# Kernel tuning notes

Hardware: AMD Instinct MI355X
Metric: run time of the kernel (lower is better)

Reference implementation:

```python
import jax, jax.numpy as jnp
import numpy as np
import math

EMBED = 1024
N_HEAD = 16
T_LEN = 2048
BATCH = 2
MLP_MULT = 4
EPS = 1e-5


def setup_inputs() -> dict:
    key = jax.random.key(0)
    ks = jax.random.split(key, 12)
    d = EMBED
    h = MLP_MULT * d
    s = 0.02
    return {
        "x": jax.random.normal(ks[0], (BATCH, T_LEN, d), dtype=jnp.float32),
        "ln1_scale": jnp.ones((d,), jnp.float32),
        "ln1_shift": jnp.zeros((d,), jnp.float32),
        "w_qkv": jax.random.normal(ks[1], (d, 3 * d), jnp.float32) * s,
        "b_qkv": jnp.zeros((3 * d,), jnp.float32),
        "ln2_scale": jnp.ones((d,), jnp.float32),
        "ln2_shift": jnp.zeros((d,), jnp.float32),
        "w_fc": jax.random.normal(ks[2], (d, h), jnp.float32) * s,
        "b_fc": jnp.zeros((h,), jnp.float32),
        "w_proj": jax.random.normal(ks[3], (h, d), jnp.float32) * s,
        "b_proj": jnp.zeros((d,), jnp.float32),
    }


def _layer_norm(x, scale, shift):
    mu = jnp.mean(x, axis=-1, keepdims=True)
    var = jnp.var(x, axis=-1, keepdims=True)
    return (x - mu) * jax.lax.rsqrt(var + EPS) * scale + shift


def _attention(h, w_qkv, b_qkv):
    B, T, C = h.shape
    hd = C // N_HEAD
    qkv = h @ w_qkv + b_qkv  # [B,T,3C]
    q, k, v = jnp.split(qkv, 3, axis=-1)
    q = q.reshape(B, T, N_HEAD, hd)
    k = k.reshape(B, T, N_HEAD, hd)
    v = v.reshape(B, T, N_HEAD, hd)
    scores = jnp.einsum("bthd,bshd->bhts", q, k) * (1.0 / math.sqrt(hd))
    causal = jnp.tril(jnp.ones((T, T), dtype=bool))
    scores = jnp.where(causal[None, None], scores, -jnp.inf)
    probs = jax.nn.softmax(scores, axis=-1)
    y = jnp.einsum("bhts,bshd->bthd", probs, v)
    return y.reshape(B, T, C)


def reference(x, ln1_scale, ln1_shift, w_qkv, b_qkv, ln2_scale, ln2_shift,
              w_fc, b_fc, w_proj, b_proj):
    x = x + _attention(_layer_norm(x, ln1_scale, ln1_shift), w_qkv, b_qkv)
    h = _layer_norm(x, ln2_scale, ln2_shift)
    # note: module names it 'gelu' but it's nn.ReLU()
    h = jax.nn.relu(h @ w_fc + b_fc) @ w_proj + b_proj
    return x + h
```

## Files before the change

kernel.cpp:

```cpp
#include <hip/hip_runtime.h>
#include <hip/hip_bf16.h>


typedef __bf16  bf16x8  __attribute__((ext_vector_type(8)));
typedef __bf16  bf16x4  __attribute__((ext_vector_type(4)));
typedef float   floatx4 __attribute__((ext_vector_type(4)));

#define T_LEN 2048
#define EMB   1024
#define NH    16
#define HD    64
#define HID   4096

#define GLOBAL_LOAD_LDS16(gp, lp) \
    __builtin_amdgcn_global_load_lds( \
        (const __attribute__((address_space(1))) void*)(gp), \
        (__attribute__((address_space(3))) void*)(lp), 16, 0, 0)

__global__ void transpose_all(const float* __restrict__ w_qkv, __bf16* __restrict__ o_qkv,
                              const float* __restrict__ w_fc,  __bf16* __restrict__ o_fc,
                              const float* __restrict__ w_pj,  __bf16* __restrict__ o_pj) {
    __shared__ float tile[32][33];
    int bid = blockIdx.x;
    const float* in; __bf16* out; int R, C, bx, by;
    if (bid < 3072)      { in = w_qkv; out = o_qkv; R = 1024; C = 3072;
                           int r = bid;        bx = r % 96;  by = r / 96;  }
    else if (bid < 7168) { in = w_fc;  out = o_fc;  R = 1024; C = 4096;
                           int r = bid - 3072; bx = r % 128; by = r / 128; }
    else                 { in = w_pj;  out = o_pj;  R = 4096; C = 1024;
                           int r = bid - 7168; bx = r % 32;  by = r / 32;  }
    int bc = bx * 32, br = by * 32;
    int tx = threadIdx.x, ty = threadIdx.y;
    for (int i = 0; i < 32; i += 8)
        tile[ty + i][tx] = in[(size_t)(br + ty + i) * C + bc + tx];
    __syncthreads();
    for (int i = 0; i < 32; i += 8) {
        int c = bc + ty + i, r = br + tx;
        out[(size_t)c * R + r] = (__bf16)tile[tx][ty + i];
    }
}

__global__ __launch_bounds__(256)
void ln_kernel(const float* __restrict__ in, const float* __restrict__ sc,
               const float* __restrict__ sh, __bf16* __restrict__ out) {
    int row = blockIdx.x;
    const float* p = in + (size_t)row * EMB;
    int tid = threadIdx.x;
    int lane = tid & 63, wave = tid >> 6;
    float v[4];
    float s = 0.f, s2 = 0.f;
    for (int j = 0; j < 4; j++) {
        v[j] = p[tid + j * 256];
        s += v[j]; s2 += v[j] * v[j];
    }
    for (int m = 1; m < 64; m <<= 1) {
        s  += __shfl_xor(s, m);
        s2 += __shfl_xor(s2, m);
    }
    __shared__ float ssum[4], ssum2[4];
    if (lane == 0) { ssum[wave] = s; ssum2[wave] = s2; }
    __syncthreads();
    float tot  = ssum[0] + ssum[1] + ssum[2] + ssum[3];
    float tot2 = ssum2[0] + ssum2[1] + ssum2[2] + ssum2[3];
    float mean = tot * (1.f / EMB);
    float var  = tot2 * (1.f / EMB) - mean * mean;
    float rstd = rsqrtf(var + 1e-5f);
    for (int j = 0; j < 4; j++) {
        int c = tid + j * 256;
        out[(size_t)row * EMB + c] = (__bf16)((v[j] - mean) * rstd * sc[c] + sh[c]);
    }
}

__global__ __launch_bounds__(512)
void gemm256(const __bf16* __restrict__ A, const __bf16* __restrict__ Bt,
             const float* __restrict__ bias, const float* __restrict__ res,
             float* __restrict__ outF, __bf16* __restrict__ outB,
             int M, int N, int lda, int KL, int relu, int gx, int gz) {
    __shared__ __align__(16) __bf16 sA[2][256][64];
    __shared__ __align__(16) __bf16 sB[2][256][64];
    const int BUFE = 256 * 64;
    int tid  = threadIdx.x;
    int lane = tid & 63, wave = tid >> 6;
    int quad = lane >> 4, l16 = lane & 15;

    int i  = blockIdx.x;
    int c  = i & 7, m = i >> 3;
    int bx = m % gx;
    int p  = (m / gx) * 8 + c;
    int by = p / gz;
    int bz = p - by * gz;

    int bm = by * 256, bn = bx * 256;
    size_t k0 = (size_t)bz * KL;
    int wm = (wave >> 2) * 128, wn = (wave & 3) * 64;

    floatx4 acc[8][4] = {};

    int srow  = tid >> 3;
    int sslot = (tid & 7) ^ (srow & 7);
    const __bf16* gA = A  + (size_t)(bm + srow) * lda + k0 + sslot * 8;
    const __bf16* gB = Bt + (size_t)(bn + srow) * lda + k0 + sslot * 8;
    __bf16* lA = &sA[0][0][0] + wave * 512;
    __bf16* lB = &sB[0][0][0] + wave * 512;
    const size_t rstep = (size_t)64 * lda;

#define STAGE256(nb, ko) do { \
    GLOBAL_LOAD_LDS16(gA + (ko),             lA + (nb) * BUFE); \
    GLOBAL_LOAD_LDS16(gB + (ko),             lB + (nb) * BUFE); \
    GLOBAL_LOAD_LDS16(gA + (ko) + rstep,     lA + (nb) * BUFE + 4096); \
    GLOBAL_LOAD_LDS16(gB + (ko) + rstep,     lB + (nb) * BUFE + 4096); \
    GLOBAL_LOAD_LDS16(gA + (ko) + 2 * rstep, lA + (nb) * BUFE + 8192); \
    GLOBAL_LOAD_LDS16(gB + (ko) + 2 * rstep, lB + (nb) * BUFE + 8192); \
    GLOBAL_LOAD_LDS16(gA + (ko) + 3 * rstep, lA + (nb) * BUFE + 12288); \
    GLOBAL_LOAD_LDS16(gB + (ko) + 3 * rstep, lB + (nb) * BUFE + 12288); \
} while (0)

#define PHASE_BAR_IN()  do { __builtin_amdgcn_s_barrier(); \
    asm volatile("s_waitcnt lgkmcnt(0)" ::: "memory"); \
    __builtin_amdgcn_sched_barrier(0); } while (0)
#define PHASE_BAR_OUT() do { __builtin_amdgcn_s_barrier(); \
    asm volatile("" ::: "memory"); } while (0)

    STAGE256(0, (size_t)0);

    int xs0  = ((quad) ^ (l16 & 7)) * 8;
    int xs1  = ((4 + quad) ^ (l16 & 7)) * 8;
    int aoff = (wm + l16) * 64;
    int boff = (wn + l16) * 64;

    const int nt = KL / 64;
    for (int t = 0; t < nt; ++t) {
        const int cur = t & 1;
        __builtin_amdgcn_s_barrier();
        asm volatile("" ::: "memory");
        if (t + 1 < nt) {
            STAGE256(cur ^ 1, (size_t)(t + 1) * 64);
            asm volatile("s_waitcnt vmcnt(8)" ::: "memory");
        } else {
            asm volatile("s_waitcnt vmcnt(0)" ::: "memory");
        }
        __builtin_amdgcn_s_barrier();
        asm volatile("" ::: "memory");
        __builtin_amdgcn_sched_barrier(0);

        const __bf16* sAc = &sA[0][0][0] + cur * BUFE;
        const __bf16* sBc = &sB[0][0][0] + cur * BUFE;

        bf16x8 a0[4][2], a1[4][2], b0[2][2], b1[2][2];

        #pragma unroll
        for (int mi = 0; mi < 4; ++mi) {
            a0[mi][0] = *(const bf16x8*)(sAc + aoff + mi * 1024 + xs0);
            a0[mi][1] = *(const bf16x8*)(sAc + aoff + mi * 1024 + xs1);
        }
        #pragma unroll
        for (int nj = 0; nj < 2; ++nj) {
            b0[nj][0] = *(const bf16x8*)(sBc + boff + nj * 1024 + xs0);
            b0[nj][1] = *(const bf16x8*)(sBc + boff + nj * 1024 + xs1);
        }
        PHASE_BAR_IN();
        __builtin_amdgcn_s_setprio(1);
        #pragma unroll
        for (int ks = 0; ks < 2; ++ks)
            #pragma unroll
            for (int mi = 0; mi < 4; ++mi)
                #pragma unroll
                for (int nj = 0; nj < 2; ++nj)
                    acc[mi][nj] = __builtin_amdgcn_mfma_f32_16x16x32_bf16(
                        a0[mi][ks], b0[nj][ks], acc[mi][nj], 0, 0, 0);
        __builtin_amdgcn_s_setprio(0);
        PHASE_BAR_OUT();

        #pragma unroll
        for (int nj = 0; nj < 2; ++nj) {
            b1[nj][0] = *(const bf16x8*)(sBc + boff + (2 + nj) * 1024 + xs0);
            b1[nj][1] = *(const bf16x8*)(sBc + boff + (2 + nj) * 1024 + xs1);
        }
        PHASE_BAR_IN();
        __builtin_amdgcn_s_setprio(1);
        #pragma unroll
        for (int ks = 0; ks < 2; ++ks)
            #pragma unroll
            for (int mi = 0; mi < 4; ++mi)
                #pragma unroll
                for (int nj = 0; nj < 2; ++nj)
                    acc[mi][2 + nj] = __builtin_amdgcn_mfma_f32_16x16x32_bf16(
                        a0[mi][ks], b1[nj][ks], acc[mi][2 + nj], 0, 0, 0);
        __builtin_amdgcn_s_setprio(0);
        PHASE_BAR_OUT();

        #pragma unroll
        for (int mi = 0; mi < 4; ++mi) {
            a1[mi][0] = *(const bf16x8*)(sAc + aoff + (4 + mi) * 1024 + xs0);
            a1[mi][1] = *(const bf16x8*)(sAc + aoff + (4 + mi) * 1024 + xs1);
        }
        PHASE_BAR_IN();
        __builtin_amdgcn_s_setprio(1);
        #pragma unroll
        for (int ks = 0; ks < 2; ++ks)
            #pragma unroll
            for (int mi = 0; mi < 4; ++mi)
                #pragma unroll
                for (int nj = 0; nj < 2; ++nj)
                    acc[4 + mi][2 + nj] = __builtin_amdgcn_mfma_f32_16x16x32_bf16(
                        a1[mi][ks], b1[nj][ks], acc[4 + mi][2 + nj], 0, 0, 0);
        __builtin_amdgcn_s_setprio(0);
        PHASE_BAR_OUT();

        __builtin_amdgcn_s_setprio(1);
        #pragma unroll
        for (int ks = 0; ks < 2; ++ks)
            #pragma unroll
            for (int mi = 0; mi < 4; ++mi)
                #pragma unroll
                for (int nj = 0; nj < 2; ++nj)
                    acc[4 + mi][nj] = __builtin_amdgcn_mfma_f32_16x16x32_bf16(
                        a1[mi][ks], b0[nj][ks], acc[4 + mi][nj], 0, 0, 0);
        __builtin_amdgcn_s_setprio(0);
    }
#undef STAGE256
#undef PHASE_BAR_IN
#undef PHASE_BAR_OUT

    if (bias) {
        #pragma unroll
        for (int mi = 0; mi < 8; ++mi) {
            int row0 = bm + wm + mi * 16 + quad * 4;
            #pragma unroll
            for (int nj = 0; nj < 4; ++nj) {
                int col = bn + wn + nj * 16 + l16;
                float bv = bias[col];
                #pragma unroll
                for (int r = 0; r < 4; ++r) {
                    size_t idx = (size_t)(row0 + r) * N + col;
                    float cc = acc[mi][nj][r] + bv;
                    if (relu) cc = fmaxf(cc, 0.f);
                    if (res)  cc += res[idx];
                    if (outF) outF[idx] = cc;
                    if (outB) outB[idx] = (__bf16)cc;
                }
            }
        }
    } else {
        __bf16* po = outB + (size_t)bz * M * N;
        #pragma unroll
        for (int mi = 0; mi < 8; ++mi) {
            int row0 = bm + wm + mi * 16 + quad * 4;
            #pragma unroll
            for (int nj = 0; nj < 4; ++nj) {
                int col = bn + wn + nj * 16 + l16;
                #pragma unroll
                for (int r = 0; r < 4; ++r)
                    po[(size_t)(row0 + r) * N + col] = (__bf16)acc[mi][nj][r];
            }
        }
    }
}

__global__ __launch_bounds__(256)
void reduce_proj(const __bf16* __restrict__ pbuf, const float* __restrict__ x2,
                 const float* __restrict__ bias, float* __restrict__ out) {
    const size_t MN = (size_t)4096 * 1024;
    size_t i = (size_t)blockIdx.x * 256 + threadIdx.x;
    float4 r = ((const float4*)x2)[i];
    float4 bb = ((const float4*)bias)[i & 255];
    float acc0 = r.x + bb.x, acc1 = r.y + bb.y;
    float acc2 = r.z + bb.z, acc3 = r.w + bb.w;
    for (int k = 0; k < 4; k++) {
        bf16x4 pv = *(const bf16x4*)&pbuf[k * MN + i * 4];
        acc0 += (float)pv[0]; acc1 += (float)pv[1];
        acc2 += (float)pv[2]; acc3 += (float)pv[3];
    }
    float4 o = {acc0, acc1, acc2, acc3};
    ((float4*)out)[i] = o;
}

__global__ __launch_bounds__(256)
void gemm_bt_n64(const __bf16* __restrict__ A, const __bf16* __restrict__ Bt,
                 const float* __restrict__ bias, const float* __restrict__ res,
                 float* __restrict__ outF, __bf16* __restrict__ outB,
                 int M, int N, int K, int relu) {
    __shared__ __align__(16) __bf16 sA[128][40];
    __shared__ __align__(16) __bf16 sB[64][40];
    int tid  = threadIdx.x;
    int lane = tid & 63, wave = tid >> 6;
    int quad = lane >> 4, l16 = lane & 15;
    int bm = blockIdx.y * 128, bn = blockIdx.x * 64;
    int wm = (wave & 1) * 64, wn = (wave >> 1) * 32;
    floatx4 acc[4][2] = {};

    int srow = tid >> 2;
    int scol = (tid & 3) * 8;
    const __bf16* gA = &A[(size_t)(bm + srow) * K + scol];
    const __bf16* gB = &Bt[(size_t)(bn + srow) * K + scol];

    uint4 ra0 = *(const uint4*)gA;
    uint4 ra1 = *(const uint4*)(gA + (size_t)64 * K);
    uint4 rb0 = *(const uint4*)gB;

    for (int kk = 0; kk < K; kk += 32) {
        __syncthreads();
        *(uint4*)&sA[srow][scol]      = ra0;
        *(uint4*)&sA[srow + 64][scol] = ra1;
        *(uint4*)&sB[srow][scol]      = rb0;
        __syncthreads();
        {
            int kn = (kk + 32 < K) ? kk + 32 : kk;
            ra0 = *(const uint4*)(gA + kn);
            ra1 = *(const uint4*)(gA + kn + (size_t)64 * K);
            rb0 = *(const uint4*)(gB + kn);
        }
        bf16x8 af[4], bfr[2];
        for (int i = 0; i < 4; i++)
            af[i] = *(const bf16x8*)&sA[wm + i * 16 + l16][quad * 8];
        for (int j = 0; j < 2; j++)
            bfr[j] = *(const bf16x8*)&sB[wn + j * 16 + l16][quad * 8];
        for (int i = 0; i < 4; i++)
            for (int j = 0; j < 2; j++)
                acc[i][j] = __builtin_amdgcn_mfma_f32_16x16x32_bf16(
                    af[i], bfr[j], acc[i][j], 0, 0, 0);
    }

    for (int i = 0; i < 4; i++) {
        int row0 = bm + wm + i * 16 + quad * 4;
        for (int j = 0; j < 2; j++) {
            int col = bn + wn + j * 16 + l16;
            float bv = bias[col];
            for (int r = 0; r < 4; r++) {
                size_t idx = (size_t)(row0 + r) * N + col;
                float c = acc[i][j][r] + bv;
                if (relu) c = fmaxf(c, 0.f);
                if (res)  c += res[idx];
                if (outF) outF[idx] = c;
                if (outB) outB[idx] = (__bf16)c;
            }
        }
    }
}

__global__ __launch_bounds__(512)
void attn_kernel(const __bf16* __restrict__ qkv, const float* __restrict__ x,
                 float* __restrict__ x2) {
    __shared__ __align__(16) __bf16 sK[2][64][72];
    __shared__ __align__(16) __bf16 sVt[2][64][72];
    __shared__ __align__(16) __bf16 sP[8][16][72];
    const int tid  = threadIdx.x;
    const int lane = tid & 63, wave = tid >> 6;
    const int quad = lane >> 4, l16 = lane & 15;

    int i = blockIdx.x;
    int c = i & 7, m = i >> 3;
    const int bh   = (m & 3) * 8 + c;
    const int qt_h = 31 - (m >> 2);
    const int h    = bh & (NH - 1);
    const int b    = bh >> 4;
    const size_t rowbase = (size_t)b * T_LEN;

    const int g  = wave >> 2;
    const int wg = wave & 3;
    const int qt = g ? (31 - qt_h) : qt_h;
    const int qrow = qt * 64 + wg * 16;
    const int dt   = qt;

    const float kQScale = 0.125f * 1.44269504088896f;
    bf16x8 ones;
    for (int j = 0; j < 8; j++) ones[j] = (__bf16)1.0f;

    const int key0 = tid >> 3, m8 = tid & 7;
    const __bf16* kp0 = qkv + (rowbase + key0) * 3072 + h * HD + m8 * 8 + 1024;
    const int pc0 = ((key0 >> 3) ^ m8) * 8 + (key0 & 7);

    bf16x8 qf[2];
    for (int ks = 0; ks < 2; ks++) {
        bf16x8 raw = *(const bf16x8*)&qkv[(rowbase + qrow + l16) * 3072
                                          + h * HD + ks * 32 + quad * 8];
        for (int j = 0; j < 8; j++)
            qf[ks][j] = (__bf16)((float)raw[j] * kQScale);
    }

    floatx4 o[4] = {}, ol = {};

    const int ntiles = qt_h + 1;
    const size_t TSTEP = (size_t)64 * 3072;

    uint4 kr0 = *(const uint4*)kp0;
    uint4 vr0 = *(const uint4*)(kp0 + 1024);
    {
        *(uint4*)&sK[0][key0][m8 * 8] = kr0;
        bf16x8 v0 = *(bf16x8*)&vr0;
        for (int j = 0; j < 8; j++) sVt[0][m8 * 8 + j][pc0] = v0[j];
    }
    kr0 = *(const uint4*)(kp0 + TSTEP);
    vr0 = *(const uint4*)(kp0 + TSTEP + 1024);
    __syncthreads();

    for (int kt = 0; kt < ntiles; kt++) {
        const int cur = kt & 1, nxt = cur ^ 1;
        if (kt + 1 < ntiles) {
            *(uint4*)&sK[nxt][key0][m8 * 8] = kr0;
            bf16x8 v0 = *(bf16x8*)&vr0;
            for (int j = 0; j < 8; j++) sVt[nxt][m8 * 8 + j][pc0] = v0[j];
            size_t offn = (size_t)((kt + 2 < ntiles) ? kt + 2 : kt + 1) * TSTEP;
            kr0 = *(const uint4*)(kp0 + offn);
            vr0 = *(const uint4*)(kp0 + offn + 1024);
        }

        if (kt <= dt) {
            floatx4 s_acc[4] = {};
            for (int jt = 0; jt < 4; jt++)
                for (int ks = 0; ks < 2; ks++) {
                    bf16x8 kf = *(const bf16x8*)&sK[cur][jt * 16 + l16]
                                                  [ks * 32 + quad * 8];
                    s_acc[jt] = __builtin_amdgcn_mfma_f32_16x16x32_bf16(
                        qf[ks], kf, s_acc[jt], 0, 0, 0);
                }

            if (kt == dt) {
                const int tq0 = qrow + quad * 4;
                const int k0 = kt * 64;
                for (int jt = 0; jt < 4; jt++) {
                    int key = k0 + jt * 16 + l16;
                    for (int r = 0; r < 4; r++) {
                        float sv = (key <= tq0 + r) ? s_acc[jt][r] : -1e30f;
                        float pv = __builtin_amdgcn_exp2f(fminf(sv, 30.f));
                        sP[wave][quad * 4 + r][jt * 16 + l16] = (__bf16)pv;
                    }
                }
            } else {
                for (int jt = 0; jt < 4; jt++)
                    for (int r = 0; r < 4; r++) {
                        float pv = __builtin_amdgcn_exp2f(fminf(s_acc[jt][r], 30.f));
                        sP[wave][quad * 4 + r][jt * 16 + l16] = (__bf16)pv;
                    }
            }

            for (int kp = 0; kp < 2; kp++) {
                bf16x8 pf = *(const bf16x8*)&sP[wave][l16][kp * 32 + quad * 8];
                ol = __builtin_amdgcn_mfma_f32_16x16x32_bf16(pf, ones, ol, 0, 0, 0);
                for (int jt2 = 0; jt2 < 4; jt2++) {
                    int d = jt2 * 16 + l16;
                    int pg = (kp * 4 + quad) ^ (d >> 3);
                    bf16x8 vf = *(const bf16x8*)&sVt[cur][d][pg * 8];
                    o[jt2] = __builtin_amdgcn_mfma_f32_16x16x32_bf16(
                        pf, vf, o[jt2], 0, 0, 0);
                }
            }
        }
        __syncthreads();
    }

    float inv[4];
    for (int r = 0; r < 4; r++) inv[r] = __builtin_amdgcn_rcpf(ol[r]);
    for (int jt2 = 0; jt2 < 4; jt2++) {
        for (int r = 0; r < 4; r++) {
            int tq  = qrow + quad * 4 + r;
            int col = h * HD + jt2 * 16 + l16;
            size_t gi = (rowbase + tq) * EMB + col;
            x2[gi] = x[gi] + o[jt2][r] * inv[r];
        }
    }
}

extern "C" void kernel_launch(void* const* d_in, const int* in_sizes, int n_in,
                              void* d_out, int out_size, void* d_ws, size_t ws_size,
                              hipStream_t stream) {
    const float* x      = (const float*)d_in[0];
    const float* ln1_s  = (const float*)d_in[1];
    const float* ln1_b  = (const float*)d_in[2];
    const float* w_qkv  = (const float*)d_in[3];
    const float* b_qkv  = (const float*)d_in[4];
    const float* ln2_s  = (const float*)d_in[5];
    const float* ln2_b  = (const float*)d_in[6];
    const float* w_fc   = (const float*)d_in[7];
    const float* b_fc   = (const float*)d_in[8];
    const float* w_proj = (const float*)d_in[9];
    const float* b_proj = (const float*)d_in[10];
    float* out = (float*)d_out;

    const int M = 2 * T_LEN;
    char* ws = (char*)d_ws;
    size_t off = 0;
    auto alloc = [&](size_t bytes) {
        void* p = ws + off; off += (bytes + 255) & ~(size_t)255; return p;
    };
    __bf16* wpj_t  = (__bf16*)alloc((size_t)1024 * 4096 * 2);
    float*  x2     = (float*) alloc((size_t)M * 1024 * 4);
    __bf16* hfc    = (__bf16*)alloc((size_t)M * 4096 * 2);
    size_t mark = off;
    __bf16* wqkv_t = (__bf16*)alloc((size_t)3072 * 1024 * 2);
    __bf16* wfc_t  = (__bf16*)alloc((size_t)4096 * 1024 * 2);
    __bf16* h1     = (__bf16*)alloc((size_t)M * 1024 * 2);
    __bf16* h2     = (__bf16*)alloc((size_t)M * 1024 * 2);
    __bf16* qkvb   = (__bf16*)alloc((size_t)M * 3072 * 2);
    __bf16* pbuf = (__bf16*)(ws + mark);
    size_t need = mark + (size_t)4 * M * 1024 * 2;
    bool can_split = ws_size >= need;

    dim3 tb(32, 8);
    transpose_all<<<11264, tb, 0, stream>>>(w_qkv, wqkv_t, w_fc, wfc_t,
                                            w_proj, wpj_t);

    ln_kernel<<<M, 256, 0, stream>>>(x, ln1_s, ln1_b, h1);

    gemm256<<<192, 512, 0, stream>>>(
        h1, wqkv_t, b_qkv, nullptr, nullptr, qkvb, M, 3072, 1024, 1024, 0,
        12, 1);

    attn_kernel<<<512, 512, 0, stream>>>(qkvb, x, x2);

    ln_kernel<<<M, 256, 0, stream>>>(x2, ln2_s, ln2_b, h2);

    gemm256<<<256, 512, 0, stream>>>(
        h2, wfc_t, b_fc, nullptr, nullptr, hfc, M, 4096, 1024, 1024, 1,
        16, 1);

    if (can_split) {
        gemm256<<<256, 512, 0, stream>>>(
            hfc, wpj_t, nullptr, nullptr, nullptr, pbuf, M, 1024, 4096, 1024, 0,
            4, 4);
        reduce_proj<<<(M * 1024 / 4) / 256, 256, 0, stream>>>(
            pbuf, x2, b_proj, out);
    } else {
        gemm_bt_n64<<<dim3(1024 / 64, M / 128), 256, 0, stream>>>(
            hfc, wpj_t, b_proj, x2, out, nullptr, M, 1024, 4096, 0);
    }
}
```

Before: 314.5 us.

## Replace 256x256 phased GEMM with simpler 128x128 tile, K-step 32 kernel

Swaps the 256x256-tile, 512-thread GEMM and its four-phase barrier/priority scheduling for a 128x128-tile, 256-thread kernel with a 32-wide K step and a new swizzled LDS layout. All three GEMM launches now use four times as many blocks. The aim is better occupancy and load balance across the CUs for these matrix sizes. In exchange there is less data reuse per tile, twice as many K iterations with barriers, and the fine-grained MFMA/LDS interleaving is gone.

```diff
diff --git a/kernel.cpp b/kernel.cpp
--- a/kernel.cpp
+++ b/kernel.cpp
@@ -71,14 +71,13 @@
     }
 }
 
-__global__ __launch_bounds__(512)
-void gemm256(const __bf16* __restrict__ A, const __bf16* __restrict__ Bt,
+__global__ __launch_bounds__(256)
+void gemm128(const __bf16* __restrict__ A, const __bf16* __restrict__ Bt,
              const float* __restrict__ bias, const float* __restrict__ res,
              float* __restrict__ outF, __bf16* __restrict__ outB,
              int M, int N, int lda, int KL, int relu, int gx, int gz) {
-    __shared__ __align__(16) __bf16 sA[2][256][64];
-    __shared__ __align__(16) __bf16 sB[2][256][64];
-    const int BUFE = 256 * 64;
+    __shared__ __align__(16) __bf16 sA[2][4096];
+    __shared__ __align__(16) __bf16 sB[2][4096];
     int tid  = threadIdx.x;
     int lane = tid & 63, wave = tid >> 6;
     int quad = lane >> 4, l16 = lane & 15;
@@ -90,141 +89,70 @@
     int by = p / gz;
     int bz = p - by * gz;
 
-    int bm = by * 256, bn = bx * 256;
+    int bm = by * 128, bn = bx * 128;
     size_t k0 = (size_t)bz * KL;
-    int wm = (wave >> 2) * 128, wn = (wave & 3) * 64;
-
-    floatx4 acc[8][4] = {};
-
-    int srow  = tid >> 3;
-    int sslot = (tid & 7) ^ (srow & 7);
-    const __bf16* gA = A  + (size_t)(bm + srow) * lda + k0 + sslot * 8;
-    const __bf16* gB = Bt + (size_t)(bn + srow) * lda + k0 + sslot * 8;
-    __bf16* lA = &sA[0][0][0] + wave * 512;
-    __bf16* lB = &sB[0][0][0] + wave * 512;
+    int wm = (wave & 1) * 64, wn = (wave >> 1) * 64;
+
+    floatx4 acc[4][4] = {};
+
+    int prow  = tid >> 3, pslot = tid & 7;
+    int sw    = pslot ^ (prow & 7);
+    int srowg = 2 * prow + (sw >> 2);
+    int scolg = (sw & 3) * 8;
+    const __bf16* gA = A  + (size_t)(bm + srowg) * lda + k0 + scolg;
+    const __bf16* gB = Bt + (size_t)(bn + srowg) * lda + k0 + scolg;
+    __bf16* lA = &sA[0][0] + tid * 8;
+    __bf16* lB = &sB[0][0] + tid * 8;
     const size_t rstep = (size_t)64 * lda;
 
-#define STAGE256(nb, ko) do { \
-    GLOBAL_LOAD_LDS16(gA + (ko),             lA + (nb) * BUFE); \
-    GLOBAL_LOAD_LDS16(gB + (ko),             lB + (nb) * BUFE); \
-    GLOBAL_LOAD_LDS16(gA + (ko) + rstep,     lA + (nb) * BUFE + 4096); \
-    GLOBAL_LOAD_LDS16(gB + (ko) + rstep,     lB + (nb) * BUFE + 4096); \
-    GLOBAL_LOAD_LDS16(gA + (ko) + 2 * rstep, lA + (nb) * BUFE + 8192); \
-    GLOBAL_LOAD_LDS16(gB + (ko) + 2 * rstep, lB + (nb) * BUFE + 8192); \
-    GLOBAL_LOAD_LDS16(gA + (ko) + 3 * rstep, lA + (nb) * BUFE + 12288); \
-    GLOBAL_LOAD_LDS16(gB + (ko) + 3 * rstep, lB + (nb) * BUFE + 12288); \
+#define STAGE128(nb, ko) do { \
+    GLOBAL_LOAD_LDS16(gA + (ko),         lA + (nb) * 4096); \
+    GLOBAL_LOAD_LDS16(gB + (ko),         lB + (nb) * 4096); \
+    GLOBAL_LOAD_LDS16(gA + (ko) + rstep, lA + (nb) * 4096 + 2048); \
+    GLOBAL_LOAD_LDS16(gB + (ko) + rstep, lB + (nb) * 4096 + 2048); \
 } while (0)
 
-#define PHASE_BAR_IN()  do { __builtin_amdgcn_s_barrier(); \
-    asm volatile("s_waitcnt lgkmcnt(0)" ::: "memory"); \
-    __builtin_amdgcn_sched_barrier(0); } while (0)
-#define PHASE_BAR_OUT() do { __builtin_amdgcn_s_barrier(); \
-    asm volatile("" ::: "memory"); } while (0)
-
-    STAGE256(0, (size_t)0);
-
-    int xs0  = ((quad) ^ (l16 & 7)) * 8;
-    int xs1  = ((4 + quad) ^ (l16 & 7)) * 8;
-    int aoff = (wm + l16) * 64;
-    int boff = (wn + l16) * 64;
-
-    const int nt = KL / 64;
+    STAGE128(0, (size_t)0);
+
+    int psl  = ((l16 & 1) * 4 + quad) ^ ((l16 >> 1) & 7);
+    int aoff = wm * 32 + (l16 >> 1) * 64 + psl * 8;
+    int boff = wn * 32 + (l16 >> 1) * 64 + psl * 8;
+
+    const int nt = KL / 32;
     for (int t = 0; t < nt; ++t) {
         const int cur = t & 1;
         __builtin_amdgcn_s_barrier();
         asm volatile("" ::: "memory");
         if (t + 1 < nt) {
-            STAGE256(cur ^ 1, (size_t)(t + 1) * 64);
-            asm volatile("s_waitcnt vmcnt(8)" ::: "memory");
+            STAGE128(cur ^ 1, (size_t)(t + 1) * 32);
+            asm volatile("s_waitcnt vmcnt(4)" ::: "memory");
         } else {
             asm volatile("s_waitcnt vmcnt(0)" ::: "memory");
         }
         __builtin_amdgcn_s_barrier();
         asm volatile("" ::: "memory");
-        __builtin_amdgcn_sched_barrier(0);
-
-        const __bf16* sAc = &sA[0][0][0] + cur * BUFE;
-        const __bf16* sBc = &sB[0][0][0] + cur * BUFE;
-
-        bf16x8 a0[4][2], a1[4][2], b0[2][2], b1[2][2];
-
+
+        const __bf16* sAc = &sA[cur][0];
+        const __bf16* sBc = &sB[cur][0];
+        bf16x8 af[4], bfr[4];
+        #pragma unroll
+        for (int mi = 0; mi < 4; ++mi)
+            af[mi] = *(const bf16x8*)(sAc + aoff + mi * 512);
+        #pragma unroll
+        for (int nj = 0; nj < 4; ++nj)
+            bfr[nj] = *(const bf16x8*)(sBc + boff + nj * 512);
+        #pragma unroll
+        for (int mi = 0; mi < 4; ++mi)
+            #pragma unroll
+            for (int nj = 0; nj < 4; ++nj)
+                acc[mi][nj] = __builtin_amdgcn_mfma_f32_16x16x32_bf16(
+                    af[mi], bfr[nj], acc[mi][nj], 0, 0, 0);
+    }
+#undef STAGE128
+
+    if (bias) {
         #pragma unroll
         for (int mi = 0; mi < 4; ++mi) {
-            a0[mi][0] = *(const bf16x8*)(sAc + aoff + mi * 1024 + xs0);
-            a0[mi][1] = *(const bf16x8*)(sAc + aoff + mi * 1024 + xs1);
-        }
-        #pragma unroll
-        for (int nj = 0; nj < 2; ++nj) {
-            b0[nj][0] = *(const bf16x8*)(sBc + boff + nj * 1024 + xs0);
-            b0[nj][1] = *(const bf16x8*)(sBc + boff + nj * 1024 + xs1);
-        }
-        PHASE_BAR_IN();
-        __builtin_amdgcn_s_setprio(1);
-        #pragma unroll
-        for (int ks = 0; ks < 2; ++ks)
-            #pragma unroll
-            for (int mi = 0; mi < 4; ++mi)
-                #pragma unroll
-                for (int nj = 0; nj < 2; ++nj)
-                    acc[mi][nj] = __builtin_amdgcn_mfma_f32_16x16x32_bf16(
-                        a0[mi][ks], b0[nj][ks], acc[mi][nj], 0, 0, 0);
-        __builtin_amdgcn_s_setprio(0);
-        PHASE_BAR_OUT();
-
-        #pragma unroll
-        for (int nj = 0; nj < 2; ++nj) {
-            b1[nj][0] = *(const bf16x8*)(sBc + boff + (2 + nj) * 1024 + xs0);
-            b1[nj][1] = *(const bf16x8*)(sBc + boff + (2 + nj) * 1024 + xs1);
-        }
-        PHASE_BAR_IN();
-        __builtin_amdgcn_s_setprio(1);
-        #pragma unroll
-        for (int ks = 0; ks < 2; ++ks)
-            #pragma unroll
-            for (int mi = 0; mi < 4; ++mi)
-                #pragma unroll
-                for (int nj = 0; nj < 2; ++nj)
-                    acc[mi][2 + nj] = __builtin_amdgcn_mfma_f32_16x16x32_bf16(
-                        a0[mi][ks], b1[nj][ks], acc[mi][2 + nj], 0, 0, 0);
-        __builtin_amdgcn_s_setprio(0);
-        PHASE_BAR_OUT();
-
-        #pragma unroll
-        for (int mi = 0; mi < 4; ++mi) {
-            a1[mi][0] = *(const bf16x8*)(sAc + aoff + (4 + mi) * 1024 + xs0);
-            a1[mi][1] = *(const bf16x8*)(sAc + aoff + (4 + mi) * 1024 + xs1);
-        }
-        PHASE_BAR_IN();
-        __builtin_amdgcn_s_setprio(1);
-        #pragma unroll
-        for (int ks = 0; ks < 2; ++ks)
-            #pragma unroll
-            for (int mi = 0; mi < 4; ++mi)
-                #pragma unroll
-                for (int nj = 0; nj < 2; ++nj)
-                    acc[4 + mi][2 + nj] = __builtin_amdgcn_mfma_f32_16x16x32_bf16(
-                        a1[mi][ks], b1[nj][ks], acc[4 + mi][2 + nj], 0, 0, 0);
-        __builtin_amdgcn_s_setprio(0);
-        PHASE_BAR_OUT();
-
-        __builtin_amdgcn_s_setprio(1);
-        #pragma unroll
-        for (int ks = 0; ks < 2; ++ks)
-            #pragma unroll
-            for (int mi = 0; mi < 4; ++mi)
-                #pragma unroll
-                for (int nj = 0; nj < 2; ++nj)
-                    acc[4 + mi][nj] = __builtin_amdgcn_mfma_f32_16x16x32_bf16(
-                        a1[mi][ks], b0[nj][ks], acc[4 + mi][nj], 0, 0, 0);
-        __builtin_amdgcn_s_setprio(0);
-    }
-#undef STAGE256
-#undef PHASE_BAR_IN
-#undef PHASE_BAR_OUT
-
-    if (bias) {
-        #pragma unroll
-        for (int mi = 0; mi < 8; ++mi) {
             int row0 = bm + wm + mi * 16 + quad * 4;
             #pragma unroll
             for (int nj = 0; nj < 4; ++nj) {
@@ -244,7 +172,7 @@
     } else {
         __bf16* po = outB + (size_t)bz * M * N;
         #pragma unroll
-        for (int mi = 0; mi < 8; ++mi) {
+        for (int mi = 0; mi < 4; ++mi) {
             int row0 = bm + wm + mi * 16 + quad * 4;
             #pragma unroll
             for (int nj = 0; nj < 4; ++nj) {
@@ -502,22 +430,22 @@
 
     ln_kernel<<<M, 256, 0, stream>>>(x, ln1_s, ln1_b, h1);
 
-    gemm256<<<192, 512, 0, stream>>>(
+    gemm128<<<768, 256, 0, stream>>>(
         h1, wqkv_t, b_qkv, nullptr, nullptr, qkvb, M, 3072, 1024, 1024, 0,
-        12, 1);
+        24, 1);
 
     attn_kernel<<<512, 512, 0, stream>>>(qkvb, x, x2);
 
     ln_kernel<<<M, 256, 0, stream>>>(x2, ln2_s, ln2_b, h2);
 
-    gemm256<<<256, 512, 0, stream>>>(
+    gemm128<<<1024, 256, 0, stream>>>(
         h2, wfc_t, b_fc, nullptr, nullptr, hfc, M, 4096, 1024, 1024, 1,
-        16, 1);
+        32, 1);
 
     if (can_split) {
-        gemm256<<<256, 512, 0, stream>>>(
+        gemm128<<<1024, 256, 0, stream>>>(
             hfc, wpj_t, nullptr, nullptr, nullptr, pbuf, M, 1024, 4096, 1024, 0,
-            4, 4);
+            8, 4);
         reduce_proj<<<(M * 1024 / 4) / 256, 256, 0, stream>>>(
             pbuf, x2, b_proj, out);
     } else {
```

After: 322.5 us. +2.6%, slower.

## Software-pipeline attention QK with triple-buffered K/V; drop GEMM phase barriers

Applied to the files above, without the earlier changes.

Attention now keeps three K/V LDS buffers and computes the next tile's QK^T scores while the current tile's softmax and PV run. Global loads are issued two tiles ahead and stored after compute. The aim is to hide LDS and MFMA latency across tiles, at the cost of extra LDS and registers. The GEMM also drops its intra-iteration phase barriers and lgkmcnt waits, leaving the compiler to schedule LDS reads against MFMAs.

```diff
diff --git a/kernel.cpp b/kernel.cpp
--- a/kernel.cpp
+++ b/kernel.cpp
@@ -115,12 +115,6 @@
     GLOBAL_LOAD_LDS16(gB + (ko) + 3 * rstep, lB + (nb) * BUFE + 12288); \
 } while (0)
 
-#define PHASE_BAR_IN()  do { __builtin_amdgcn_s_barrier(); \
-    asm volatile("s_waitcnt lgkmcnt(0)" ::: "memory"); \
-    __builtin_amdgcn_sched_barrier(0); } while (0)
-#define PHASE_BAR_OUT() do { __builtin_amdgcn_s_barrier(); \
-    asm volatile("" ::: "memory"); } while (0)
-
     STAGE256(0, (size_t)0);
 
     int xs0  = ((quad) ^ (l16 & 7)) * 8;
@@ -158,7 +152,6 @@
             b0[nj][0] = *(const bf16x8*)(sBc + boff + nj * 1024 + xs0);
             b0[nj][1] = *(const bf16x8*)(sBc + boff + nj * 1024 + xs1);
         }
-        PHASE_BAR_IN();
         __builtin_amdgcn_s_setprio(1);
         #pragma unroll
         for (int ks = 0; ks < 2; ++ks)
@@ -169,14 +162,12 @@
                     acc[mi][nj] = __builtin_amdgcn_mfma_f32_16x16x32_bf16(
                         a0[mi][ks], b0[nj][ks], acc[mi][nj], 0, 0, 0);
         __builtin_amdgcn_s_setprio(0);
-        PHASE_BAR_OUT();
 
         #pragma unroll
         for (int nj = 0; nj < 2; ++nj) {
             b1[nj][0] = *(const bf16x8*)(sBc + boff + (2 + nj) * 1024 + xs0);
             b1[nj][1] = *(const bf16x8*)(sBc + boff + (2 + nj) * 1024 + xs1);
         }
-        PHASE_BAR_IN();
         __builtin_amdgcn_s_setprio(1);
         #pragma unroll
         for (int ks = 0; ks < 2; ++ks)
@@ -187,14 +178,12 @@
                     acc[mi][2 + nj] = __builtin_amdgcn_mfma_f32_16x16x32_bf16(
                         a0[mi][ks], b1[nj][ks], acc[mi][2 + nj], 0, 0, 0);
         __builtin_amdgcn_s_setprio(0);
-        PHASE_BAR_OUT();
 
         #pragma unroll
         for (int mi = 0; mi < 4; ++mi) {
             a1[mi][0] = *(const bf16x8*)(sAc + aoff + (4 + mi) * 1024 + xs0);
             a1[mi][1] = *(const bf16x8*)(sAc + aoff + (4 + mi) * 1024 + xs1);
         }
-        PHASE_BAR_IN();
         __builtin_amdgcn_s_setprio(1);
         #pragma unroll
         for (int ks = 0; ks < 2; ++ks)
@@ -205,7 +194,6 @@
                     acc[4 + mi][2 + nj] = __builtin_amdgcn_mfma_f32_16x16x32_bf16(
                         a1[mi][ks], b1[nj][ks], acc[4 + mi][2 + nj], 0, 0, 0);
         __builtin_amdgcn_s_setprio(0);
-        PHASE_BAR_OUT();
 
         __builtin_amdgcn_s_setprio(1);
         #pragma unroll
@@ -219,8 +207,6 @@
         __builtin_amdgcn_s_setprio(0);
     }
 #undef STAGE256
-#undef PHASE_BAR_IN
-#undef PHASE_BAR_OUT
 
     if (bias) {
         #pragma unroll
@@ -341,8 +327,8 @@
 __global__ __launch_bounds__(512)
 void attn_kernel(const __bf16* __restrict__ qkv, const float* __restrict__ x,
                  float* __restrict__ x2) {
-    __shared__ __align__(16) __bf16 sK[2][64][72];
-    __shared__ __align__(16) __bf16 sVt[2][64][72];
+    __shared__ __align__(16) __bf16 sK[3][64][72];
+    __shared__ __align__(16) __bf16 sVt[3][64][72];
     __shared__ __align__(16) __bf16 sP[8][16][72];
     const int tid  = threadIdx.x;
     const int lane = tid & 63, wave = tid >> 6;
@@ -379,74 +365,109 @@
     }
 
     floatx4 o[4] = {}, ol = {};
+    floatx4 sn[4] = {};
 
     const int ntiles = qt_h + 1;
     const size_t TSTEP = (size_t)64 * 3072;
 
-    uint4 kr0 = *(const uint4*)kp0;
-    uint4 vr0 = *(const uint4*)(kp0 + 1024);
+    uint4 kr = *(const uint4*)kp0;
+    uint4 vr = *(const uint4*)(kp0 + 1024);
     {
-        *(uint4*)&sK[0][key0][m8 * 8] = kr0;
-        bf16x8 v0 = *(bf16x8*)&vr0;
+        *(uint4*)&sK[0][key0][m8 * 8] = kr;
+        bf16x8 v0 = *(bf16x8*)&vr;
         for (int j = 0; j < 8; j++) sVt[0][m8 * 8 + j][pc0] = v0[j];
     }
-    kr0 = *(const uint4*)(kp0 + TSTEP);
-    vr0 = *(const uint4*)(kp0 + TSTEP + 1024);
+    kr = *(const uint4*)(kp0 + TSTEP);
+    vr = *(const uint4*)(kp0 + TSTEP + 1024);
+    {
+        *(uint4*)&sK[1][key0][m8 * 8] = kr;
+        bf16x8 v1 = *(bf16x8*)&vr;
+        for (int j = 0; j < 8; j++) sVt[1][m8 * 8 + j][pc0] = v1[j];
+    }
     __syncthreads();
 
+    #pragma unroll
+    for (int jt = 0; jt < 4; jt++)
+        #pragma unroll
+        for (int ks = 0; ks < 2; ks++) {
+            bf16x8 kf = *(const bf16x8*)&sK[0][jt * 16 + l16][ks * 32 + quad * 8];
+            sn[jt] = __builtin_amdgcn_mfma_f32_16x16x32_bf16(
+                qf[ks], kf, sn[jt], 0, 0, 0);
+        }
+
+    int bc = 0, bn_ = 1, bs = 2;
     for (int kt = 0; kt < ntiles; kt++) {
-        const int cur = kt & 1, nxt = cur ^ 1;
-        if (kt + 1 < ntiles) {
-            *(uint4*)&sK[nxt][key0][m8 * 8] = kr0;
-            bf16x8 v0 = *(bf16x8*)&vr0;
-            for (int j = 0; j < 8; j++) sVt[nxt][m8 * 8 + j][pc0] = v0[j];
-            size_t offn = (size_t)((kt + 2 < ntiles) ? kt + 2 : kt + 1) * TSTEP;
-            kr0 = *(const uint4*)(kp0 + offn);
-            vr0 = *(const uint4*)(kp0 + offn + 1024);
+        floatx4 sc[4];
+        #pragma unroll
+        for (int jt = 0; jt < 4; jt++) {
+            sc[jt] = sn[jt];
+            sn[jt] = (floatx4){0.f, 0.f, 0.f, 0.f};
+        }
+
+        if (kt + 2 < ntiles) {
+            size_t offn = (size_t)(kt + 2) * TSTEP;
+            kr = *(const uint4*)(kp0 + offn);
+            vr = *(const uint4*)(kp0 + offn + 1024);
+        }
+
+        if (kt + 1 <= dt) {
+            #pragma unroll
+            for (int jt = 0; jt < 4; jt++)
+                #pragma unroll
+                for (int ks = 0; ks < 2; ks++) {
+                    bf16x8 kf = *(const bf16x8*)&sK[bn_][jt * 16 + l16]
+                                                  [ks * 32 + quad * 8];
+                    sn[jt] = __builtin_amdgcn_mfma_f32_16x16x32_bf16(
+                        qf[ks], kf, sn[jt], 0, 0, 0);
+                }
         }
 
         if (kt <= dt) {
-            floatx4 s_acc[4] = {};
-            for (int jt = 0; jt < 4; jt++)
-                for (int ks = 0; ks < 2; ks++) {
-                    bf16x8 kf = *(const bf16x8*)&sK[cur][jt * 16 + l16]
-                                                  [ks * 32 + quad * 8];
-                    s_acc[jt] = __builtin_amdgcn_mfma_f32_16x16x32_bf16(
-                        qf[ks], kf, s_acc[jt], 0, 0, 0);
-                }
-
             if (kt == dt) {
                 const int tq0 = qrow + quad * 4;
                 const int k0 = kt * 64;
+                #pragma unroll
                 for (int jt = 0; jt < 4; jt++) {
                     int key = k0 + jt * 16 + l16;
+                    #pragma unroll
                     for (int r = 0; r < 4; r++) {
-                        float sv = (key <= tq0 + r) ? s_acc[jt][r] : -1e30f;
+                        float sv = (key <= tq0 + r) ? sc[jt][r] : -1e30f;
                         float pv = __builtin_amdgcn_exp2f(fminf(sv, 30.f));
                         sP[wave][quad * 4 + r][jt * 16 + l16] = (__bf16)pv;
                     }
                 }
             } else {
+                #pragma unroll
                 for (int jt = 0; jt < 4; jt++)
+                    #pragma unroll
                     for (int r = 0; r < 4; r++) {
-                        float pv = __builtin_amdgcn_exp2f(fminf(s_acc[jt][r], 30.f));
+                        float pv = __builtin_amdgcn_exp2f(fminf(sc[jt][r], 30.f));
                         sP[wave][quad * 4 + r][jt * 16 + l16] = (__bf16)pv;
                     }
             }
 
+            #pragma unroll
             for (int kp = 0; kp < 2; kp++) {
                 bf16x8 pf = *(const bf16x8*)&sP[wave][l16][kp * 32 + quad * 8];
                 ol = __builtin_amdgcn_mfma_f32_16x16x32_bf16(pf, ones, ol, 0, 0, 0);
+                #pragma unroll
                 for (int jt2 = 0; jt2 < 4; jt2++) {
                     int d = jt2 * 16 + l16;
                     int pg = (kp * 4 + quad) ^ (d >> 3);
-                    bf16x8 vf = *(const bf16x8*)&sVt[cur][d][pg * 8];
+                    bf16x8 vf = *(const bf16x8*)&sVt[bc][d][pg * 8];
                     o[jt2] = __builtin_amdgcn_mfma_f32_16x16x32_bf16(
                         pf, vf, o[jt2], 0, 0, 0);
                 }
             }
         }
+
+        if (kt + 2 < ntiles) {
+            *(uint4*)&sK[bs][key0][m8 * 8] = kr;
+            bf16x8 v0 = *(bf16x8*)&vr;
+            for (int j = 0; j < 8; j++) sVt[bs][m8 * 8 + j][pc0] = v0[j];
+        }
         __syncthreads();
+        int tmp = bc; bc = bn_; bn_ = bs; bs = tmp;
     }
 
     float inv[4];
```

New measurement: 306.0 us. 1.03x faster.
